# Optimization experiments

Measured on AMD Instinct MI355X. Metric: run time of the kernel, lower is better.

## Reference

```python
import jax, jax.numpy as jnp
import numpy as np

P_DIMS = [100, 100, 80, 60, 60]
P = sum(P_DIMS)  # 400
N_STREAMS = len(P_DIMS)
MEM_ITERS = 5
DECAY = 0.8
LR = 0.5        # hebbian_learning_rate
FORGET = 0.9999 # hebbian_forget_rate
NEG_SLOPE = 0.01


def _build_masks():
    idx = np.cumsum([0] + P_DIMS)
    hier = np.zeros((P, P), np.float32)
    for i in range(N_STREAMS):
        for j in range(i, N_STREAMS):
            hier[idx[i]:idx[i + 1], idx[j]:idx[j + 1]] = 1.0
    iters = [MEM_ITERS - f for f in range(N_STREAMS)]  # [5,4,3,2,1]
    rmasks = np.zeros((MEM_ITERS, P), np.float32)
    for it in range(MEM_ITERS):
        for s, r in enumerate(iters):
            if it < r:
                rmasks[it, idx[s]:idx[s + 1]] = 1.0
    return jnp.asarray(hier), jnp.asarray(rmasks)


def setup_inputs() -> dict:
    key = jax.random.key(0)
    k1, k2, k3, k4 = jax.random.split(key, 4)
    B = 512
    return {
        'M_prev': jax.random.normal(k1, (B, P, P), dtype=jnp.float32) * 0.1,
        'p_inferred': jax.random.normal(k2, (B, P), dtype=jnp.float32),
        'p_generated': jax.random.normal(k3, (B, P), dtype=jnp.float32),
        'query': jax.random.normal(k4, (B, P), dtype=jnp.float32),
    }


def reference(M_prev, p_inferred, p_generated, query):
    hier_mask, retrieval_masks = _build_masks()

    # Hebbian update: M = clamp(forget*M_prev + lr*(p-phat)(p+phat)^T, -1, 1) * hier_mask
    outer = (p_inferred - p_generated)[:, :, None] * (p_inferred + p_generated)[:, None, :]
    M = jnp.clip(FORGET * M_prev + LR * outer, -1.0, 1.0) * hier_mask

    # Hierarchical attractor retrieval
    h = jax.nn.leaky_relu(jnp.clip(query, -1.0, 1.0), NEG_SLOPE)

    def step(h, mask):
        mv = jnp.einsum('bpq,bq->bp', M, h)
        upd = jax.nn.leaky_relu(jnp.clip(DECAY * h + mv, -1.0, 1.0), NEG_SLOPE)
        return (1.0 - mask) * h + mask * upd, None

    h, _ = jax.lax.scan(step, h, retrieval_masks)
    return h
```

## Files before the change

### kernel.cpp

```cpp
#include <hip/hip_runtime.h>


#define PDIM 400
#define CROWS 46
#define FORGET 0.9999f
#define LRATE  0.5f
#define DECAY  0.8f
#define SLOPE  0.01f

typedef float f32x2 __attribute__((ext_vector_type(2)));
union V4 { float4 f4; f32x2 h2[2]; };

__device__ __forceinline__ float leaky_clip(float x) {
    x = fminf(fmaxf(x, -1.0f), 1.0f);
    return x > 0.0f ? x : SLOPE * x;
}
__device__ __forceinline__ float clamp1(float x) {
    return fminf(fmaxf(x, -1.0f), 1.0f);
}
__device__ __forceinline__ f32x2 pk_mul(f32x2 a, f32x2 b) {
    f32x2 d;
    asm("v_pk_mul_f32 %0, %1, %2" : "=v"(d) : "v"(a), "v"(b));
    return d;
}
__device__ __forceinline__ f32x2 pk_fma(f32x2 a, f32x2 b, f32x2 c) {
    f32x2 d;
    asm("v_pk_fma_f32 %0, %1, %2, %3" : "=v"(d) : "v"(a), "v"(b), "v"(c));
    return d;
}
__device__ __forceinline__ f32x2 clamp2(f32x2 x) {
    x.x = clamp1(x.x); x.y = clamp1(x.y); return x;
}

__device__ __forceinline__ int c4beg(int p) {
    return (p < 100) ? 0 : (p < 200) ? 25 : (p < 280) ? 50 : (p < 340) ? 70 : 85;
}

__device__ __forceinline__ float wave_sum(float x) {
    x += __int_as_float(__builtin_amdgcn_update_dpp(0, __float_as_int(x), 0xB1,  0xf, 0xf, true));
    x += __int_as_float(__builtin_amdgcn_update_dpp(0, __float_as_int(x), 0x4E,  0xf, 0xf, true));
    x += __int_as_float(__builtin_amdgcn_update_dpp(0, __float_as_int(x), 0x141, 0xf, 0xf, true));
    x += __int_as_float(__builtin_amdgcn_update_dpp(0, __float_as_int(x), 0x140, 0xf, 0xf, true));
    x += __int_as_float(__builtin_amdgcn_update_dpp(0, __float_as_int(x), 0x142, 0xf, 0xf, true));
    x += __int_as_float(__builtin_amdgcn_update_dpp(0, __float_as_int(x), 0x143, 0xf, 0xf, true));
    return __int_as_float(__builtin_amdgcn_readlane(__float_as_int(x), 63));
}

__device__ __forceinline__ void load_row(const float* __restrict__ Mb,
                                         int p, int R, int l,
                                         int& c4, V4& A, V4& B) {
    A.f4 = make_float4(0.f, 0.f, 0.f, 0.f);
    B.f4 = A.f4;
    c4 = 0;
    if (p < R) {
        c4 = c4beg(p);
        const float* __restrict__ row = Mb + (size_t)p * PDIM;
        if (l >= c4)                A.f4 = *(const float4*)(row + 4 * l);
        if (l < 36 && 64 + l >= c4) B.f4 = *(const float4*)(row + 256 + 4 * l);
    }
}

__global__ __launch_bounds__(512, 4)
void hier_mem_kernel(const float* __restrict__ M_prev,
                     const float* __restrict__ p_inf,
                     const float* __restrict__ p_gen,
                     const float* __restrict__ query,
                     float* __restrict__ out)
{
    __shared__ float s_mc[CROWS][PDIM];
    __shared__ float s_h[2][PDIM];
    __shared__ float s_la[PDIM];

    const int b   = blockIdx.x;
    const int tid = threadIdx.x;
    const int l   = tid & 63;
    const int wid = tid >> 6;
    const float* __restrict__ Mb = M_prev + (size_t)b * PDIM * PDIM;

    if (tid < PDIM) {
        const float pi = p_inf[b * PDIM + tid];
        const float pg = p_gen[b * PDIM + tid];
        s_la[tid]   = LRATE * (pi - pg);
        s_h[0][tid] = leaky_clip(query[b * PDIM + tid]);
    }

    const float4 z4 = make_float4(0.f, 0.f, 0.f, 0.f);
    const float4* __restrict__ pi4 = (const float4*)(p_inf + (size_t)b * PDIM);
    const float4* __restrict__ pg4 = (const float4*)(p_gen + (size_t)b * PDIM);
    V4 vA, vB; vB.f4 = z4;
    {
        const float4 x = pi4[l], y = pg4[l];
        vA.f4 = make_float4(x.x + y.x, x.y + y.y, x.z + y.z, x.w + y.w);
        if (l < 36) {
            const float4 u = pi4[64 + l], v = pg4[64 + l];
            vB.f4 = make_float4(u.x + v.x, u.y + v.y, u.z + v.z, u.w + v.w);
        }
    }
    const f32x2 F2 = {FORGET, FORGET};
    __syncthreads();

    {
        const float* __restrict__ hcur = s_h[0];
        float* __restrict__ hnew = s_h[1];
        V4 hA, hB; hB.f4 = z4;
        hA.f4 = *(const float4*)(hcur + 4 * l);
        if (l < 36) hB.f4 = *(const float4*)(hcur + 256 + 4 * l);

        int p = wid;
        int c0, c1; V4 A0, B0, A1, B1;
        load_row(Mb, p,     PDIM, l, c0, A0, B0);
        load_row(Mb, p + 8, PDIM, l, c1, A1, B1);

        while (p < PDIM) {
            int c2; V4 A2, B2;
            load_row(Mb, p + 16, PDIM, l, c2, A2, B2);

            const float la = s_la[p];
            const f32x2 la2 = {la, la};
            f32x2 acc2 = {0.f, 0.f};
            V4 mA, mB; mA.f4 = z4; mB.f4 = z4;
            if (l >= c0) {
                mA.h2[0] = clamp2(pk_fma(F2, A0.h2[0], pk_mul(la2, vA.h2[0])));
                mA.h2[1] = clamp2(pk_fma(F2, A0.h2[1], pk_mul(la2, vA.h2[1])));
                acc2 = pk_fma(mA.h2[0], hA.h2[0], acc2);
                acc2 = pk_fma(mA.h2[1], hA.h2[1], acc2);
            }
            if (l < 36 && 64 + l >= c0) {
                mB.h2[0] = clamp2(pk_fma(F2, B0.h2[0], pk_mul(la2, vB.h2[0])));
                mB.h2[1] = clamp2(pk_fma(F2, B0.h2[1], pk_mul(la2, vB.h2[1])));
                acc2 = pk_fma(mB.h2[0], hB.h2[0], acc2);
                acc2 = pk_fma(mB.h2[1], hB.h2[1], acc2);
            }
            if (p < CROWS) {
                *(float4*)&s_mc[p][4 * l] = mA.f4;
                if (l < 36) *(float4*)&s_mc[p][256 + 4 * l] = mB.f4;
            }

            const float tot = wave_sum(acc2.x + acc2.y);
            if (l == 0) {
                hnew[p] = leaky_clip(fmaf(DECAY, hcur[p], tot));
            }

            p += 8; c0 = c1; A0 = A1; B0 = B1; c1 = c2; A1 = A2; B1 = B2;
        }
        __syncthreads();
    }

    int cur = 1;
    const int Rt[4] = {340, 280, 200, 100};
    #pragma unroll
    for (int t = 0; t < 4; ++t) {
        const int R = Rt[t];
        const float* __restrict__ hcur = s_h[cur];
        float* __restrict__ hnew = s_h[cur ^ 1];

        V4 hA, hB; hB.f4 = z4;
        hA.f4 = *(const float4*)(hcur + 4 * l);
        if (l < 36) hB.f4 = *(const float4*)(hcur + 256 + 4 * l);

        int sp = CROWS + wid;
        int c0; V4 A0, B0;
        load_row(Mb, sp, R, l, c0, A0, B0);

        {
            int p = wid;
            V4 KA, KB; KB.f4 = z4;
            KA.f4 = *(const float4*)&s_mc[p][4 * l];
            if (l < 36) KB.f4 = *(const float4*)&s_mc[p][256 + 4 * l];
            while (p < CROWS) {
                const int pn = p + 8;
                V4 NA, NB; NA.f4 = z4; NB.f4 = z4;
                if (pn < CROWS) {
                    NA.f4 = *(const float4*)&s_mc[pn][4 * l];
                    if (l < 36) NB.f4 = *(const float4*)&s_mc[pn][256 + 4 * l];
                }
                f32x2 acc2 = pk_fma(KA.h2[0], hA.h2[0],
                             pk_fma(KA.h2[1], hA.h2[1],
                             pk_fma(KB.h2[0], hB.h2[0],
                             pk_mul(KB.h2[1], hB.h2[1]))));
                const float tot = wave_sum(acc2.x + acc2.y);
                if (l == 0) {
                    hnew[p] = leaky_clip(fmaf(DECAY, hcur[p], tot));
                }
                p = pn; KA = NA; KB = NB;
            }
        }

        while (sp < R) {
            int c1n; V4 A1, B1;
            load_row(Mb, sp + 8, R, l, c1n, A1, B1);

            const float la = s_la[sp];
            const f32x2 la2 = {la, la};
            f32x2 acc2 = {0.f, 0.f};
            if (l >= c0) {
                f32x2 m0 = clamp2(pk_fma(F2, A0.h2[0], pk_mul(la2, vA.h2[0])));
                f32x2 m1 = clamp2(pk_fma(F2, A0.h2[1], pk_mul(la2, vA.h2[1])));
                acc2 = pk_fma(m0, hA.h2[0], acc2);
                acc2 = pk_fma(m1, hA.h2[1], acc2);
            }
            if (l < 36 && 64 + l >= c0) {
                f32x2 m0 = clamp2(pk_fma(F2, B0.h2[0], pk_mul(la2, vB.h2[0])));
                f32x2 m1 = clamp2(pk_fma(F2, B0.h2[1], pk_mul(la2, vB.h2[1])));
                acc2 = pk_fma(m0, hB.h2[0], acc2);
                acc2 = pk_fma(m1, hB.h2[1], acc2);
            }

            const float tot = wave_sum(acc2.x + acc2.y);
            if (l == 0) {
                hnew[sp] = leaky_clip(fmaf(DECAY, hcur[sp], tot));
            }

            sp += 8; c0 = c1n; A0 = A1; B0 = B1;
        }

        if (tid >= R && tid < PDIM) hnew[tid] = hcur[tid];
        __syncthreads();
        cur ^= 1;
    }

    if (tid < PDIM) {
        out[b * PDIM + tid] = s_h[cur][tid];
    }
}

extern "C" void kernel_launch(void* const* d_in, const int* in_sizes, int n_in,
                              void* d_out, int out_size, void* d_ws, size_t ws_size,
                              hipStream_t stream) {
    const float* M_prev = (const float*)d_in[0];
    const float* p_inf  = (const float*)d_in[1];
    const float* p_gen  = (const float*)d_in[2];
    const float* query  = (const float*)d_in[3];
    float* out = (float*)d_out;

    const int B = in_sizes[1] / PDIM;
    hipLaunchKernelGGL(hier_mem_kernel, dim3(B), dim3(512), 0, stream,
                       M_prev, p_inf, p_gen, query, out);
}
```

Before: 481.8 us.

## Cache first matrix rows in registers and deepen prefetch in later iterations

Rows 0-31 of the updated Hebbian matrix (four rows per wave) are now held in registers across the retrieval iterations. Rows 32-77 go to shared memory, and only rows from 78 onward are reloaded from global memory and recomputed. The later-iteration global row loop now prefetches two rows ahead instead of one. This cuts global re-reads of M_prev on each iteration, at the cost of more vector registers per thread. Higher register pressure could reduce occupancy under the 512x4 launch bound.

```diff
diff --git a/kernel.cpp b/kernel.cpp
--- a/kernel.cpp
+++ b/kernel.cpp
@@ -2,7 +2,9 @@
 
 
 #define PDIM 400
-#define CROWS 46
+#define RREG 4
+#define LROW0 32
+#define LROWN 78
 #define FORGET 0.9999f
 #define LRATE  0.5f
 #define DECAY  0.8f
@@ -67,7 +69,7 @@
                      const float* __restrict__ query,
                      float* __restrict__ out)
 {
-    __shared__ float s_mc[CROWS][PDIM];
+    __shared__ float s_mc[LROWN - LROW0][PDIM];
     __shared__ float s_h[2][PDIM];
     __shared__ float s_la[PDIM];
 
@@ -97,6 +99,9 @@
         }
     }
     const f32x2 F2 = {FORGET, FORGET};
+
+    V4 rA[RREG], rB[RREG];
+
     __syncthreads();
 
     {
@@ -110,6 +115,33 @@
         int c0, c1; V4 A0, B0, A1, B1;
         load_row(Mb, p,     PDIM, l, c0, A0, B0);
         load_row(Mb, p + 8, PDIM, l, c1, A1, B1);
+
+        #pragma unroll
+        for (int k = 0; k < RREG; ++k) {
+            int c2; V4 A2, B2;
+            load_row(Mb, p + 16, PDIM, l, c2, A2, B2);
+
+            const float la = s_la[p];
+            const f32x2 la2 = {la, la};
+            V4 mA, mB; mA.f4 = z4; mB.f4 = z4;
+            mA.h2[0] = clamp2(pk_fma(F2, A0.h2[0], pk_mul(la2, vA.h2[0])));
+            mA.h2[1] = clamp2(pk_fma(F2, A0.h2[1], pk_mul(la2, vA.h2[1])));
+            if (l < 36) {
+                mB.h2[0] = clamp2(pk_fma(F2, B0.h2[0], pk_mul(la2, vB.h2[0])));
+                mB.h2[1] = clamp2(pk_fma(F2, B0.h2[1], pk_mul(la2, vB.h2[1])));
+            }
+            rA[k] = mA; rB[k] = mB;
+
+            f32x2 acc2 = pk_fma(mA.h2[0], hA.h2[0],
+                         pk_fma(mA.h2[1], hA.h2[1],
+                         pk_fma(mB.h2[0], hB.h2[0],
+                         pk_mul(mB.h2[1], hB.h2[1]))));
+            const float tot = wave_sum(acc2.x + acc2.y);
+            if (l == 0) {
+                hnew[p] = leaky_clip(fmaf(DECAY, hcur[p], tot));
+            }
+            p += 8; c0 = c1; A0 = A1; B0 = B1; c1 = c2; A1 = A2; B1 = B2;
+        }
 
         while (p < PDIM) {
             int c2; V4 A2, B2;
@@ -131,9 +163,9 @@
                 acc2 = pk_fma(mB.h2[0], hB.h2[0], acc2);
                 acc2 = pk_fma(mB.h2[1], hB.h2[1], acc2);
             }
-            if (p < CROWS) {
-                *(float4*)&s_mc[p][4 * l] = mA.f4;
-                if (l < 36) *(float4*)&s_mc[p][256 + 4 * l] = mB.f4;
+            if (p < LROWN) {
+                *(float4*)&s_mc[p - LROW0][4 * l] = mA.f4;
+                if (l < 36) *(float4*)&s_mc[p - LROW0][256 + 4 * l] = mB.f4;
             }
 
             const float tot = wave_sum(acc2.x + acc2.y);
@@ -158,21 +190,35 @@
         hA.f4 = *(const float4*)(hcur + 4 * l);
         if (l < 36) hB.f4 = *(const float4*)(hcur + 256 + 4 * l);
 
-        int sp = CROWS + wid;
-        int c0; V4 A0, B0;
-        load_row(Mb, sp, R, l, c0, A0, B0);
+        int sp = LROWN + wid;
+        int c0, c1; V4 A0, B0, A1, B1;
+        load_row(Mb, sp,     R, l, c0, A0, B0);
+        load_row(Mb, sp + 8, R, l, c1, A1, B1);
+
+        #pragma unroll
+        for (int k = 0; k < RREG; ++k) {
+            const int p = wid + 8 * k;
+            f32x2 acc2 = pk_fma(rA[k].h2[0], hA.h2[0],
+                         pk_fma(rA[k].h2[1], hA.h2[1],
+                         pk_fma(rB[k].h2[0], hB.h2[0],
+                         pk_mul(rB[k].h2[1], hB.h2[1]))));
+            const float tot = wave_sum(acc2.x + acc2.y);
+            if (l == 0) {
+                hnew[p] = leaky_clip(fmaf(DECAY, hcur[p], tot));
+            }
+        }
 
         {
-            int p = wid;
+            int p = LROW0 + wid;
             V4 KA, KB; KB.f4 = z4;
-            KA.f4 = *(const float4*)&s_mc[p][4 * l];
-            if (l < 36) KB.f4 = *(const float4*)&s_mc[p][256 + 4 * l];
-            while (p < CROWS) {
+            KA.f4 = *(const float4*)&s_mc[p - LROW0][4 * l];
+            if (l < 36) KB.f4 = *(const float4*)&s_mc[p - LROW0][256 + 4 * l];
+            while (p < LROWN) {
                 const int pn = p + 8;
                 V4 NA, NB; NA.f4 = z4; NB.f4 = z4;
-                if (pn < CROWS) {
-                    NA.f4 = *(const float4*)&s_mc[pn][4 * l];
-                    if (l < 36) NB.f4 = *(const float4*)&s_mc[pn][256 + 4 * l];
+                if (pn < LROWN) {
+                    NA.f4 = *(const float4*)&s_mc[pn - LROW0][4 * l];
+                    if (l < 36) NB.f4 = *(const float4*)&s_mc[pn - LROW0][256 + 4 * l];
                 }
                 f32x2 acc2 = pk_fma(KA.h2[0], hA.h2[0],
                              pk_fma(KA.h2[1], hA.h2[1],
@@ -187,8 +233,8 @@
         }
 
         while (sp < R) {
-            int c1n; V4 A1, B1;
-            load_row(Mb, sp + 8, R, l, c1n, A1, B1);
+            int c2; V4 A2, B2;
+            load_row(Mb, sp + 16, R, l, c2, A2, B2);
 
             const float la = s_la[sp];
             const f32x2 la2 = {la, la};
@@ -211,7 +257,7 @@
                 hnew[sp] = leaky_clip(fmaf(DECAY, hcur[sp], tot));
             }
 
-            sp += 8; c0 = c1n; A0 = A1; B0 = B1;
+            sp += 8; c0 = c1; A0 = A1; B0 = B1; c1 = c2; A1 = A2; B1 = B2;
         }
 
         if (tid >= R && tid < PDIM) hnew[tid] = hcur[tid];
```

Measured after the change: 473.5 us. About the same (-1.7%).
